# Kernel tuning notes

Measured on AMD Instinct MI355X. Metric: run time of the kernel, lower is better.

The kernel has to match this reference:

```python
import jax, jax.numpy as jnp
import numpy as np

B, T, J, D = 32, 1024, 64, 256


def setup_inputs() -> dict:
    key = jax.random.key(0)
    k1, k2, k3, k4 = jax.random.split(key, 4)
    U = jax.random.normal(k1, (B, J, D), dtype=jnp.float32)
    H = jax.random.normal(k2, (B, T, D), dtype=jnp.float32)
    # similarity_layer: Linear(3*D, 1) -> weight [3*D], bias scalar
    w = jax.random.normal(k3, (3 * D,), dtype=jnp.float32) * (1.0 / np.sqrt(3 * D))
    b = jax.random.normal(k4, (), dtype=jnp.float32) * 0.01
    return {"U": U, "H": H, "w": w, "b": b}


def reference(U, H, w, b):
    # Linear([H; U; H*U]) decomposes exactly into three small contractions:
    # S[b,t,j] = H[b,t]@w_h + U[b,j]@w_u + (H[b,t]*w_hu)@U[b,j] + bias
    w_h, w_u, w_hu = w[:D], w[D:2 * D], w[2 * D:]
    S = (
        jnp.einsum("btd,d->bt", H, w_h)[:, :, None]
        + jnp.einsum("bjd,d->bj", U, w_u)[:, None, :]
        + jnp.einsum("btd,bjd->btj", H * w_hu, U)
        + b
    )  # [B, T, J]
    A = jax.nn.softmax(S, axis=2)                      # context-to-query attention
    c2q = jnp.einsum("btj,bjd->btd", A, U)             # [B, T, D]
    b_att = jax.nn.softmax(jnp.max(S, axis=2), axis=1)  # [B, T]
    q2c = jnp.einsum("bt,btd->bd", b_att, H)[:, None, :]  # [B, 1, D]
    G = jnp.concatenate((H, c2q, H * c2q, H * q2c), axis=2)  # [B, T, 4D]
    return (G, c2q, q2c)
```

## Files before the change

kernel.cpp:

```cpp
#include <hip/hip_runtime.h>
#include <hip/hip_bf16.h>

#define BB 32
#define TT 1024
#define JJ 64
#define DD 256

__global__ __launch_bounds__(256) void k0_prep(const float* __restrict__ U,
                                               const float* __restrict__ H,
                                               const float* __restrict__ w,
                                               const float* __restrict__ bp,
                                               float* __restrict__ Up,
                                               float* __restrict__ uw,
                                               float* __restrict__ hw) {
    const int wave = threadIdx.x >> 6;
    const int lane = threadIdx.x & 63;
    if (blockIdx.x < 512) {
        const int row = blockIdx.x * 4 + wave;
        float4 u   = *(const float4*)(U + (size_t)row * DD + lane * 4);
        float4 whu = *(const float4*)(w + 2 * DD + lane * 4);
        float4 wu  = *(const float4*)(w + DD + lane * 4);
        float4 o;
        o.x = u.x * whu.x; o.y = u.y * whu.y; o.z = u.z * whu.z; o.w = u.w * whu.w;
        *(float4*)(Up + (size_t)row * DD + lane * 4) = o;
        float p = fmaf(u.x, wu.x, fmaf(u.y, wu.y, fmaf(u.z, wu.z, u.w * wu.w)));
        #pragma unroll
        for (int m = 32; m >= 1; m >>= 1) p += __shfl_xor(p, m, 64);
        if (lane == 0) uw[row] = p + bp[0];
    } else {
        const int base = (blockIdx.x - 512) * 64 + wave * 16;
        float4 wh = *(const float4*)(w + lane * 4);
        float pr[16];
        #pragma unroll
        for (int r = 0; r < 16; ++r) {
            float4 h = *(const float4*)(H + (size_t)(base + r) * DD + lane * 4);
            pr[r] = fmaf(h.x, wh.x, fmaf(h.y, wh.y, fmaf(h.z, wh.z, h.w * wh.w)));
        }
        #pragma unroll
        for (int m = 32; m >= 1; m >>= 1) {
            #pragma unroll
            for (int r = 0; r < 16; ++r) pr[r] += __shfl_xor(pr[r], m, 64);
        }
        if (lane == 0) {
            #pragma unroll
            for (int r = 0; r < 16; ++r) hw[base + r] = pr[r];
        }
    }
}

__global__ __launch_bounds__(512, 4) void k1_main(const float* __restrict__ H,
                                                  const float* __restrict__ U,
                                                  const float* __restrict__ Up,
                                                  const float* __restrict__ uw,
                                                  const float* __restrict__ hw,
                                                  float* __restrict__ m_ws,
                                                  float* __restrict__ G,
                                                  float* __restrict__ c2q_out) {
    __shared__ float lds[20480];
    const int tid  = threadIdx.x;
    const int lane = tid & 63;
    const int wave = __builtin_amdgcn_readfirstlane(tid >> 6);
    const int b    = blockIdx.x >> 4;
    const int t0   = (blockIdx.x & 15) << 6;
    const int r0   = t0 + wave * 8;

    const float* Ub = Up + (size_t)b * JJ * DD;
    #pragma unroll
    for (int it = 0; it < 8; ++it) {
        const int j = it * 8 + wave;
        float4 v = *(const float4*)((const char*)Ub + j * 1024 + lane * 16);
        *(float4*)((char*)lds + j * 1024 + ((lane * 16) ^ ((j & 7) << 4))) = v;
    }
    __syncthreads();

    const float uwj = uw[b * JJ + lane];
    const int   swz = (lane & 7) << 4;
    const char* urow = (const char*)lds + lane * 1024;
    const float* Hb  = H + (size_t)b * TT * DD;

    const float* h0 = Hb + (size_t)(r0 + 0) * DD;
    const float* h1 = Hb + (size_t)(r0 + 1) * DD;
    const float* h2 = Hb + (size_t)(r0 + 2) * DD;
    const float* h3 = Hb + (size_t)(r0 + 3) * DD;
    const float* h4p = Hb + (size_t)(r0 + 4) * DD;
    const float* h5 = Hb + (size_t)(r0 + 5) * DD;
    const float* h6 = Hb + (size_t)(r0 + 6) * DD;
    const float* h7 = Hb + (size_t)(r0 + 7) * DD;
    float a0 = 0.f, a1 = 0.f, a2 = 0.f, a3 = 0.f, a4 = 0.f, a5 = 0.f, a6 = 0.f, a7 = 0.f;
    #pragma unroll 2
    for (int dc = 0; dc < 64; ++dc) {
        float4 u  = *(const float4*)(urow + ((dc * 16) ^ swz));
        float4 x0 = *(const float4*)(h0 + dc * 4);
        float4 x1 = *(const float4*)(h1 + dc * 4);
        float4 x2 = *(const float4*)(h2 + dc * 4);
        float4 x3 = *(const float4*)(h3 + dc * 4);
        float4 x4 = *(const float4*)(h4p + dc * 4);
        float4 x5 = *(const float4*)(h5 + dc * 4);
        float4 x6 = *(const float4*)(h6 + dc * 4);
        float4 x7 = *(const float4*)(h7 + dc * 4);
        a0 = fmaf(x0.x, u.x, fmaf(x0.y, u.y, fmaf(x0.z, u.z, fmaf(x0.w, u.w, a0))));
        a1 = fmaf(x1.x, u.x, fmaf(x1.y, u.y, fmaf(x1.z, u.z, fmaf(x1.w, u.w, a1))));
        a2 = fmaf(x2.x, u.x, fmaf(x2.y, u.y, fmaf(x2.z, u.z, fmaf(x2.w, u.w, a2))));
        a3 = fmaf(x3.x, u.x, fmaf(x3.y, u.y, fmaf(x3.z, u.z, fmaf(x3.w, u.w, a3))));
        a4 = fmaf(x4.x, u.x, fmaf(x4.y, u.y, fmaf(x4.z, u.z, fmaf(x4.w, u.w, a4))));
        a5 = fmaf(x5.x, u.x, fmaf(x5.y, u.y, fmaf(x5.z, u.z, fmaf(x5.w, u.w, a5))));
        a6 = fmaf(x6.x, u.x, fmaf(x6.y, u.y, fmaf(x6.z, u.z, fmaf(x6.w, u.w, a6))));
        a7 = fmaf(x7.x, u.x, fmaf(x7.y, u.y, fmaf(x7.z, u.z, fmaf(x7.w, u.w, a7))));
    }
    __syncthreads();

    const float* Ug = U + (size_t)b * JJ * DD;
    float4 st[8];
    #pragma unroll
    for (int it = 0; it < 8; ++it) {
        const int j = it * 8 + wave;
        st[it] = *(const float4*)((const char*)Ug + j * 1024 + lane * 16);
    }

    float s[8] = {a0 + uwj, a1 + uwj, a2 + uwj, a3 + uwj,
                  a4 + uwj, a5 + uwj, a6 + uwj, a7 + uwj};
    float mx[8];
    #pragma unroll
    for (int r = 0; r < 8; ++r) mx[r] = s[r];
    #pragma unroll
    for (int m = 32; m >= 1; m >>= 1) {
        #pragma unroll
        for (int r = 0; r < 8; ++r) mx[r] = fmaxf(mx[r], __shfl_xor(mx[r], m, 64));
    }
    float p[8], l[8];
    #pragma unroll
    for (int r = 0; r < 8; ++r) { p[r] = __expf(s[r] - mx[r]); l[r] = p[r]; }
    #pragma unroll
    for (int m = 32; m >= 1; m >>= 1) {
        #pragma unroll
        for (int r = 0; r < 8; ++r) l[r] += __shfl_xor(l[r], m, 64);
    }
    #pragma unroll
    for (int r = 0; r < 8; ++r)
        lds[16384 + (wave * 8 + r) * 64 + lane] = p[r] * (1.0f / l[r]);
    if (lane == 0) {
        #pragma unroll
        for (int r = 0; r < 8; ++r) m_ws[b * TT + r0 + r] = mx[r] + hw[b * TT + r0 + r];
    }

    #pragma unroll
    for (int it = 0; it < 8; ++it) {
        const int j = it * 8 + wave;
        *(float4*)((char*)lds + j * 1024 + lane * 16) = st[it];
    }
    __syncthreads();

    float4 acc[8];
    #pragma unroll
    for (int r = 0; r < 8; ++r) { acc[r].x = 0.f; acc[r].y = 0.f; acc[r].z = 0.f; acc[r].w = 0.f; }
    const float* Arow = &lds[16384 + (wave * 8) * 64];
    #pragma unroll 2
    for (int j = 0; j < 64; ++j) {
        float4 u = *(const float4*)((const char*)lds + j * 1024 + lane * 16);
        #pragma unroll
        for (int r = 0; r < 8; ++r) {
            const float aj = Arow[r * 64 + j];
            acc[r].x = fmaf(aj, u.x, acc[r].x);
            acc[r].y = fmaf(aj, u.y, acc[r].y);
            acc[r].z = fmaf(aj, u.z, acc[r].z);
            acc[r].w = fmaf(aj, u.w, acc[r].w);
        }
    }

    const size_t Gbase = (size_t)b * TT * 1024;
    #pragma unroll 1
    for (int r = 0; r < 8; ++r) {
        const int row = r0 + r;
        float4 h4 = *(const float4*)(Hb + (size_t)row * DD + lane * 4);
        float4 c  = acc[r];
        float4 hc;
        hc.x = h4.x * c.x; hc.y = h4.y * c.y; hc.z = h4.z * c.z; hc.w = h4.w * c.w;
        float* Grow = G + Gbase + (size_t)row * 1024;
        *(float4*)(Grow + lane * 4)        = h4;
        *(float4*)(Grow + 256 + lane * 4)  = c;
        *(float4*)(Grow + 512 + lane * 4)  = hc;
        *(float4*)(c2q_out + ((size_t)b * TT + row) * DD + lane * 4) = c;
    }
}

__global__ __launch_bounds__(256) void k2_batt(const float* __restrict__ m_ws,
                                               float* __restrict__ wt,
                                               float* __restrict__ q2c_out) {
    __shared__ float red[256];
    const int b = blockIdx.x, tid = threadIdx.x;
    float v0 = m_ws[b * TT + tid];
    float v1 = m_ws[b * TT + 256 + tid];
    float v2 = m_ws[b * TT + 512 + tid];
    float v3 = m_ws[b * TT + 768 + tid];
    red[tid] = fmaxf(fmaxf(v0, v1), fmaxf(v2, v3));
    __syncthreads();
    for (int s = 128; s >= 1; s >>= 1) {
        if (tid < s) red[tid] = fmaxf(red[tid], red[tid + s]);
        __syncthreads();
    }
    const float M = red[0];
    __syncthreads();
    float e0 = __expf(v0 - M), e1 = __expf(v1 - M), e2 = __expf(v2 - M), e3 = __expf(v3 - M);
    red[tid] = e0 + e1 + e2 + e3;
    __syncthreads();
    for (int s = 128; s >= 1; s >>= 1) {
        if (tid < s) red[tid] += red[tid + s];
        __syncthreads();
    }
    const float iz = 1.0f / red[0];
    wt[b * TT + tid]       = e0 * iz;
    wt[b * TT + 256 + tid] = e1 * iz;
    wt[b * TT + 512 + tid] = e2 * iz;
    wt[b * TT + 768 + tid] = e3 * iz;
    q2c_out[b * DD + tid] = 0.0f;
}

__global__ __launch_bounds__(256) void k2b_q2c(const float* __restrict__ H,
                                               const float* __restrict__ wt,
                                               float* __restrict__ q2c_out) {
    const int b = blockIdx.x >> 4, c = blockIdx.x & 15, tid = threadIdx.x;
    const float* Hb = H + ((size_t)b * TT + c * 64) * DD;
    const float* wb = wt + b * TT + c * 64;
    float acc = 0.f;
    #pragma unroll 4
    for (int i = 0; i < 64; ++i) acc = fmaf(wb[i], Hb[(size_t)i * DD + tid], acc);
    atomicAdd(&q2c_out[b * DD + tid], acc);
}

__global__ __launch_bounds__(256) void k3_gtail(const float* __restrict__ H,
                                                const float* __restrict__ q2c,
                                                float* __restrict__ G) {
    const size_t idx = (size_t)blockIdx.x * 256 + threadIdx.x;
    const int d4 = (int)(idx & 63);
    const size_t bt = idx >> 6;
    const int b = (int)(bt >> 10);
    float4 h = *(const float4*)(H + idx * 4);
    float4 q = *(const float4*)(q2c + (size_t)b * DD + d4 * 4);
    float4 o;
    o.x = h.x * q.x; o.y = h.y * q.y; o.z = h.z * q.z; o.w = h.w * q.w;
    *(float4*)(G + bt * 1024 + 768 + d4 * 4) = o;
}

extern "C" void kernel_launch(void* const* d_in, const int* in_sizes, int n_in,
                              void* d_out, int out_size, void* d_ws, size_t ws_size,
                              hipStream_t stream) {
    const float* U  = (const float*)d_in[0];
    const float* H  = (const float*)d_in[1];
    const float* w  = (const float*)d_in[2];
    const float* bp = (const float*)d_in[3];
    float* out = (float*)d_out;

    float* G       = out;
    float* c2q_out = out + (size_t)BB * TT * 4 * DD;
    float* q2c_out = c2q_out + (size_t)BB * TT * DD;

    float* Up   = (float*)d_ws;
    float* uwp  = Up + (size_t)BB * JJ * DD;
    float* m_ws = uwp + BB * JJ;
    float* wtp  = m_ws + BB * TT;
    float* hwp  = wtp + BB * TT;

    k0_prep<<<1024, 256, 0, stream>>>(U, H, w, bp, Up, uwp, hwp);
    k1_main<<<BB * (TT / 64), 512, 0, stream>>>(H, U, Up, uwp, hwp, m_ws, G, c2q_out);
    k2_batt<<<BB, 256, 0, stream>>>(m_ws, wtp, q2c_out);
    k2b_q2c<<<BB * 16, 256, 0, stream>>>(H, wtp, q2c_out);
    k3_gtail<<<BB * TT * DD / 4 / 256, 256, 0, stream>>>(H, q2c_out, G);
}
```

Measured before the change: 284.7 us.

## Halve k1 tile and LDS, split D into prefetched halves, use nontemporal stores

The main kernel now processes 32 time rows per block instead of 64, and stages U in two 128-column halves. The next half is prefetched into registers while the current half is computed, which cuts LDS use from 80KB to 40KB and raises the occupancy target from 4 to 6. G and c2q outputs, including the gtail kernel, are written with nontemporal stores to avoid polluting the cache, and the q2c reduction uses twice as many blocks over half the rows. The cost is extra barriers and twice as many blocks re-loading U per batch.

After: 300.9 us. +5.7%, slower.

```diff
diff --git a/kernel.cpp b/kernel.cpp
--- a/kernel.cpp
+++ b/kernel.cpp
@@ -5,6 +5,13 @@
 #define TT 1024
 #define JJ 64
 #define DD 256
+
+typedef __attribute__((ext_vector_type(4))) float f32x4;
+__device__ __forceinline__ void nt_store4(float* addr, float4 v) {
+    union { float4 a; f32x4 b; } u;
+    u.a = v;
+    __builtin_nontemporal_store(u.b, (f32x4*)addr);
+}
 
 __global__ __launch_bounds__(256) void k0_prep(const float* __restrict__ U,
                                                const float* __restrict__ H,
@@ -48,7 +55,7 @@
     }
 }
 
-__global__ __launch_bounds__(512, 4) void k1_main(const float* __restrict__ H,
+__global__ __launch_bounds__(512, 6) void k1_main(const float* __restrict__ H,
                                                   const float* __restrict__ U,
                                                   const float* __restrict__ Up,
                                                   const float* __restrict__ uw,
@@ -56,131 +63,144 @@
                                                   float* __restrict__ m_ws,
                                                   float* __restrict__ G,
                                                   float* __restrict__ c2q_out) {
-    __shared__ float lds[20480];
+    __shared__ float lds[10240];
+    float* Abuf = lds + 8192;
     const int tid  = threadIdx.x;
     const int lane = tid & 63;
     const int wave = __builtin_amdgcn_readfirstlane(tid >> 6);
-    const int b    = blockIdx.x >> 4;
-    const int t0   = (blockIdx.x & 15) << 6;
-    const int r0   = t0 + wave * 8;
-
+    const int b    = blockIdx.x >> 5;
+    const int t0   = (blockIdx.x & 31) << 5;
+    const int r0   = t0 + wave * 4;
+    const float* Hb = H  + (size_t)b * TT * DD;
     const float* Ub = Up + (size_t)b * JJ * DD;
+    const float* Ug = U  + (size_t)b * JJ * DD;
+    const float uwj = uw[b * JJ + lane];
+
+    float4 pf[4];
+    float s0 = 0.f, s1 = 0.f, s2 = 0.f, s3 = 0.f;
+
+    #define PF_LOAD(SRC, HBYTE)                                                          \
+        { _Pragma("unroll") for (int i = 0; i < 4; ++i) {                                \
+            int idx = i * 512 + tid; int row = idx >> 5, q = idx & 31;                   \
+            pf[i] = *(const float4*)((const char*)(SRC) + row * 1024 + (HBYTE) + q * 16); } }
+    #define PF_STORE()                                                                   \
+        { _Pragma("unroll") for (int i = 0; i < 4; ++i) {                                \
+            int idx = i * 512 + tid; int row = idx >> 5, q = idx & 31;                   \
+            *(float4*)((char*)lds + row * 512 + ((q * 16) ^ ((row & 7) << 4))) = pf[i]; } }
+
     #pragma unroll
-    for (int it = 0; it < 8; ++it) {
-        const int j = it * 8 + wave;
-        float4 v = *(const float4*)((const char*)Ub + j * 1024 + lane * 16);
-        *(float4*)((char*)lds + j * 1024 + ((lane * 16) ^ ((j & 7) << 4))) = v;
-    }
-    __syncthreads();
-
-    const float uwj = uw[b * JJ + lane];
-    const int   swz = (lane & 7) << 4;
-    const char* urow = (const char*)lds + lane * 1024;
-    const float* Hb  = H + (size_t)b * TT * DD;
-
-    const float* h0 = Hb + (size_t)(r0 + 0) * DD;
-    const float* h1 = Hb + (size_t)(r0 + 1) * DD;
-    const float* h2 = Hb + (size_t)(r0 + 2) * DD;
-    const float* h3 = Hb + (size_t)(r0 + 3) * DD;
-    const float* h4p = Hb + (size_t)(r0 + 4) * DD;
-    const float* h5 = Hb + (size_t)(r0 + 5) * DD;
-    const float* h6 = Hb + (size_t)(r0 + 6) * DD;
-    const float* h7 = Hb + (size_t)(r0 + 7) * DD;
-    float a0 = 0.f, a1 = 0.f, a2 = 0.f, a3 = 0.f, a4 = 0.f, a5 = 0.f, a6 = 0.f, a7 = 0.f;
-    #pragma unroll 2
-    for (int dc = 0; dc < 64; ++dc) {
-        float4 u  = *(const float4*)(urow + ((dc * 16) ^ swz));
-        float4 x0 = *(const float4*)(h0 + dc * 4);
-        float4 x1 = *(const float4*)(h1 + dc * 4);
-        float4 x2 = *(const float4*)(h2 + dc * 4);
-        float4 x3 = *(const float4*)(h3 + dc * 4);
-        float4 x4 = *(const float4*)(h4p + dc * 4);
-        float4 x5 = *(const float4*)(h5 + dc * 4);
-        float4 x6 = *(const float4*)(h6 + dc * 4);
-        float4 x7 = *(const float4*)(h7 + dc * 4);
-        a0 = fmaf(x0.x, u.x, fmaf(x0.y, u.y, fmaf(x0.z, u.z, fmaf(x0.w, u.w, a0))));
-        a1 = fmaf(x1.x, u.x, fmaf(x1.y, u.y, fmaf(x1.z, u.z, fmaf(x1.w, u.w, a1))));
-        a2 = fmaf(x2.x, u.x, fmaf(x2.y, u.y, fmaf(x2.z, u.z, fmaf(x2.w, u.w, a2))));
-        a3 = fmaf(x3.x, u.x, fmaf(x3.y, u.y, fmaf(x3.z, u.z, fmaf(x3.w, u.w, a3))));
-        a4 = fmaf(x4.x, u.x, fmaf(x4.y, u.y, fmaf(x4.z, u.z, fmaf(x4.w, u.w, a4))));
-        a5 = fmaf(x5.x, u.x, fmaf(x5.y, u.y, fmaf(x5.z, u.z, fmaf(x5.w, u.w, a5))));
-        a6 = fmaf(x6.x, u.x, fmaf(x6.y, u.y, fmaf(x6.z, u.z, fmaf(x6.w, u.w, a6))));
-        a7 = fmaf(x7.x, u.x, fmaf(x7.y, u.y, fmaf(x7.z, u.z, fmaf(x7.w, u.w, a7))));
-    }
-    __syncthreads();
-
-    const float* Ug = U + (size_t)b * JJ * DD;
-    float4 st[8];
-    #pragma unroll
-    for (int it = 0; it < 8; ++it) {
-        const int j = it * 8 + wave;
-        st[it] = *(const float4*)((const char*)Ug + j * 1024 + lane * 16);
-    }
-
-    float s[8] = {a0 + uwj, a1 + uwj, a2 + uwj, a3 + uwj,
-                  a4 + uwj, a5 + uwj, a6 + uwj, a7 + uwj};
-    float mx[8];
-    #pragma unroll
-    for (int r = 0; r < 8; ++r) mx[r] = s[r];
-    #pragma unroll
-    for (int m = 32; m >= 1; m >>= 1) {
-        #pragma unroll
-        for (int r = 0; r < 8; ++r) mx[r] = fmaxf(mx[r], __shfl_xor(mx[r], m, 64));
-    }
-    float p[8], l[8];
-    #pragma unroll
-    for (int r = 0; r < 8; ++r) { p[r] = __expf(s[r] - mx[r]); l[r] = p[r]; }
-    #pragma unroll
-    for (int m = 32; m >= 1; m >>= 1) {
-        #pragma unroll
-        for (int r = 0; r < 8; ++r) l[r] += __shfl_xor(l[r], m, 64);
-    }
-    #pragma unroll
-    for (int r = 0; r < 8; ++r)
-        lds[16384 + (wave * 8 + r) * 64 + lane] = p[r] * (1.0f / l[r]);
-    if (lane == 0) {
-        #pragma unroll
-        for (int r = 0; r < 8; ++r) m_ws[b * TT + r0 + r] = mx[r] + hw[b * TT + r0 + r];
-    }
-
-    #pragma unroll
-    for (int it = 0; it < 8; ++it) {
-        const int j = it * 8 + wave;
-        *(float4*)((char*)lds + j * 1024 + lane * 16) = st[it];
-    }
-    __syncthreads();
-
-    float4 acc[8];
-    #pragma unroll
-    for (int r = 0; r < 8; ++r) { acc[r].x = 0.f; acc[r].y = 0.f; acc[r].z = 0.f; acc[r].w = 0.f; }
-    const float* Arow = &lds[16384 + (wave * 8) * 64];
-    #pragma unroll 2
-    for (int j = 0; j < 64; ++j) {
-        float4 u = *(const float4*)((const char*)lds + j * 1024 + lane * 16);
-        #pragma unroll
-        for (int r = 0; r < 8; ++r) {
-            const float aj = Arow[r * 64 + j];
-            acc[r].x = fmaf(aj, u.x, acc[r].x);
-            acc[r].y = fmaf(aj, u.y, acc[r].y);
-            acc[r].z = fmaf(aj, u.z, acc[r].z);
-            acc[r].w = fmaf(aj, u.w, acc[r].w);
-        }
-    }
+    for (int i = 0; i < 4; ++i) {
+        int idx = i * 512 + tid; int row = idx >> 5, q = idx & 31;
+        float4 v = *(const float4*)((const char*)Ub + row * 1024 + q * 16);
+        *(float4*)((char*)lds + row * 512 + ((q * 16) ^ ((row & 7) << 4))) = v;
+    }
+    __syncthreads();
+
+    #define S_HALF(HOFF_F)                                                               \
+        { const float* hp0 = Hb + (size_t)(r0 + 0) * DD + (HOFF_F);                      \
+          const float* hp1 = Hb + (size_t)(r0 + 1) * DD + (HOFF_F);                      \
+          const float* hp2 = Hb + (size_t)(r0 + 2) * DD + (HOFF_F);                      \
+          const float* hp3 = Hb + (size_t)(r0 + 3) * DD + (HOFF_F);                      \
+          asm volatile("" : "+v"(hp0), "+v"(hp1), "+v"(hp2), "+v"(hp3));                 \
+          const char* ur = (const char*)lds + lane * 512;                                \
+          const int swz = (lane & 7) << 4;                                               \
+          _Pragma("unroll 2") for (int dc = 0; dc < 32; ++dc) {                          \
+              float4 u  = *(const float4*)(ur + ((dc * 16) ^ swz));                      \
+              float4 x0 = *(const float4*)(hp0 + dc * 4);                                \
+              float4 x1 = *(const float4*)(hp1 + dc * 4);                                \
+              float4 x2 = *(const float4*)(hp2 + dc * 4);                                \
+              float4 x3 = *(const float4*)(hp3 + dc * 4);                                \
+              s0 = fmaf(x0.x, u.x, fmaf(x0.y, u.y, fmaf(x0.z, u.z, fmaf(x0.w, u.w, s0))));\
+              s1 = fmaf(x1.x, u.x, fmaf(x1.y, u.y, fmaf(x1.z, u.z, fmaf(x1.w, u.w, s1))));\
+              s2 = fmaf(x2.x, u.x, fmaf(x2.y, u.y, fmaf(x2.z, u.z, fmaf(x2.w, u.w, s2))));\
+              s3 = fmaf(x3.x, u.x, fmaf(x3.y, u.y, fmaf(x3.z, u.z, fmaf(x3.w, u.w, s3))));\
+          } }
+
+    PF_LOAD(Ub, 512);
+    S_HALF(0);
+    __syncthreads();
+    PF_STORE();
+    __syncthreads();
+
+    PF_LOAD(Ug, 0);
+    S_HALF(128);
+    {
+        float sv0 = s0 + uwj, sv1 = s1 + uwj, sv2 = s2 + uwj, sv3 = s3 + uwj;
+        float m0 = sv0, m1 = sv1, m2 = sv2, m3 = sv3;
+        #pragma unroll
+        for (int m = 32; m >= 1; m >>= 1) {
+            m0 = fmaxf(m0, __shfl_xor(m0, m, 64));
+            m1 = fmaxf(m1, __shfl_xor(m1, m, 64));
+            m2 = fmaxf(m2, __shfl_xor(m2, m, 64));
+            m3 = fmaxf(m3, __shfl_xor(m3, m, 64));
+        }
+        float p0 = __expf(sv0 - m0), p1 = __expf(sv1 - m1);
+        float p2 = __expf(sv2 - m2), p3 = __expf(sv3 - m3);
+        float l0 = p0, l1 = p1, l2 = p2, l3 = p3;
+        #pragma unroll
+        for (int m = 32; m >= 1; m >>= 1) {
+            l0 += __shfl_xor(l0, m, 64);
+            l1 += __shfl_xor(l1, m, 64);
+            l2 += __shfl_xor(l2, m, 64);
+            l3 += __shfl_xor(l3, m, 64);
+        }
+        Abuf[(wave * 4 + 0) * 64 + lane] = p0 * (1.0f / l0);
+        Abuf[(wave * 4 + 1) * 64 + lane] = p1 * (1.0f / l1);
+        Abuf[(wave * 4 + 2) * 64 + lane] = p2 * (1.0f / l2);
+        Abuf[(wave * 4 + 3) * 64 + lane] = p3 * (1.0f / l3);
+        if (lane == 0) {
+            float4 mm;
+            mm.x = m0 + hw[b * TT + r0 + 0];
+            mm.y = m1 + hw[b * TT + r0 + 1];
+            mm.z = m2 + hw[b * TT + r0 + 2];
+            mm.w = m3 + hw[b * TT + r0 + 3];
+            *(float4*)(m_ws + b * TT + r0) = mm;
+        }
+    }
+    __syncthreads();
+    PF_STORE();
+    __syncthreads();
 
     const size_t Gbase = (size_t)b * TT * 1024;
-    #pragma unroll 1
-    for (int r = 0; r < 8; ++r) {
-        const int row = r0 + r;
-        float4 h4 = *(const float4*)(Hb + (size_t)row * DD + lane * 4);
-        float4 c  = acc[r];
-        float4 hc;
-        hc.x = h4.x * c.x; hc.y = h4.y * c.y; hc.z = h4.z * c.z; hc.w = h4.w * c.w;
-        float* Grow = G + Gbase + (size_t)row * 1024;
-        *(float4*)(Grow + lane * 4)        = h4;
-        *(float4*)(Grow + 256 + lane * 4)  = c;
-        *(float4*)(Grow + 512 + lane * 4)  = hc;
-        *(float4*)(c2q_out + ((size_t)b * TT + row) * DD + lane * 4) = c;
-    }
+
+    #define C2Q_HALF(HOFF_F)                                                             \
+        { const int q = lane & 31, rh = lane >> 5;                                       \
+          float4 a0 = {0.f,0.f,0.f,0.f}, a1 = {0.f,0.f,0.f,0.f};                         \
+          const float* Ar0 = Abuf + (wave * 4 + rh) * 64;                                \
+          const float* Ar1 = Ar0 + 128;                                                  \
+          _Pragma("unroll 2") for (int j = 0; j < 64; ++j) {                             \
+              float4 u = *(const float4*)((const char*)lds + j * 512 +                   \
+                                          ((q * 16) ^ ((j & 7) << 4)));                  \
+              float w0 = Ar0[j], w1 = Ar1[j];                                            \
+              a0.x = fmaf(w0, u.x, a0.x); a0.y = fmaf(w0, u.y, a0.y);                    \
+              a0.z = fmaf(w0, u.z, a0.z); a0.w = fmaf(w0, u.w, a0.w);                    \
+              a1.x = fmaf(w1, u.x, a1.x); a1.y = fmaf(w1, u.y, a1.y);                    \
+              a1.z = fmaf(w1, u.z, a1.z); a1.w = fmaf(w1, u.w, a1.w);                    \
+          }                                                                              \
+          _Pragma("unroll") for (int k = 0; k < 2; ++k) {                                \
+              const int row = r0 + rh + 2 * k;                                           \
+              float4 c = k ? a1 : a0;                                                    \
+              float4 h4 = *(const float4*)(Hb + (size_t)row * DD + (HOFF_F) + q * 4);    \
+              float4 hc; hc.x = h4.x * c.x; hc.y = h4.y * c.y;                           \
+              hc.z = h4.z * c.z; hc.w = h4.w * c.w;                                      \
+              float* Grow = G + Gbase + (size_t)row * 1024 + (HOFF_F) + q * 4;           \
+              nt_store4(Grow,       h4);                                                 \
+              nt_store4(Grow + 256, c);                                                  \
+              nt_store4(Grow + 512, hc);                                                 \
+              nt_store4(c2q_out + ((size_t)b * TT + row) * DD + (HOFF_F) + q * 4, c);    \
+          } }
+
+    PF_LOAD(Ug, 512);
+    C2Q_HALF(0);
+    __syncthreads();
+    PF_STORE();
+    __syncthreads();
+    C2Q_HALF(128);
+
+    #undef PF_LOAD
+    #undef PF_STORE
+    #undef S_HALF
+    #undef C2Q_HALF
 }
 
 __global__ __launch_bounds__(256) void k2_batt(const float* __restrict__ m_ws,
@@ -218,12 +238,13 @@
 __global__ __launch_bounds__(256) void k2b_q2c(const float* __restrict__ H,
                                                const float* __restrict__ wt,
                                                float* __restrict__ q2c_out) {
-    const int b = blockIdx.x >> 4, c = blockIdx.x & 15, tid = threadIdx.x;
-    const float* Hb = H + ((size_t)b * TT + c * 64) * DD;
-    const float* wb = wt + b * TT + c * 64;
+    const int b = blockIdx.x >> 5, c = blockIdx.x & 31, tid = threadIdx.x;
+    const float* Hb = H + ((size_t)b * TT + c * 32) * DD;
+    const float* wb = wt + b * TT + c * 32;
+    asm volatile("" : "+v"(wb));
     float acc = 0.f;
-    #pragma unroll 4
-    for (int i = 0; i < 64; ++i) acc = fmaf(wb[i], Hb[(size_t)i * DD + tid], acc);
+    #pragma unroll 8
+    for (int i = 0; i < 32; ++i) acc = fmaf(wb[i], Hb[(size_t)i * DD + tid], acc);
     atomicAdd(&q2c_out[b * DD + tid], acc);
 }
 
@@ -238,7 +259,7 @@
     float4 q = *(const float4*)(q2c + (size_t)b * DD + d4 * 4);
     float4 o;
     o.x = h.x * q.x; o.y = h.y * q.y; o.z = h.z * q.z; o.w = h.w * q.w;
-    *(float4*)(G + bt * 1024 + 768 + d4 * 4) = o;
+    nt_store4(G + bt * 1024 + 768 + d4 * 4, o);
 }
 
 extern "C" void kernel_launch(void* const* d_in, const int* in_sizes, int n_in,
@@ -261,8 +282,8 @@
     float* hwp  = wtp + BB * TT;
 
     k0_prep<<<1024, 256, 0, stream>>>(U, H, w, bp, Up, uwp, hwp);
-    k1_main<<<BB * (TT / 64), 512, 0, stream>>>(H, U, Up, uwp, hwp, m_ws, G, c2q_out);
+    k1_main<<<BB * (TT / 32), 512, 0, stream>>>(H, U, Up, uwp, hwp, m_ws, G, c2q_out);
     k2_batt<<<BB, 256, 0, stream>>>(m_ws, wtp, q2c_out);
-    k2b_q2c<<<BB * 16, 256, 0, stream>>>(H, wtp, q2c_out);
+    k2b_q2c<<<BB * 32, 256, 0, stream>>>(H, wtp, q2c_out);
     k3_gtail<<<BB * TT * DD / 4 / 256, 256, 0, stream>>>(H, q2c_out, G);
 }
```
